# Optimization experiments

Measured on AMD Instinct MI355X. Metric: run time of the kernel, lower is better.

## Reference

```python
import jax, jax.numpy as jnp
import numpy as np

D = 1024      # d_model
H = 16        # num_heads
DH = D // H   # head_dim = 64
BASE = 10000.0


def setup_inputs() -> dict:
    key = jax.random.key(0)
    ks = jax.random.split(key, 5)
    lengths = np.array([1024, 768, 896, 1024], dtype=np.int32)
    cu = np.concatenate([[0], np.cumsum(lengths)]).astype(np.int32)
    T = int(cu[-1])  # 3712 packed tokens
    x = jax.random.normal(ks[0], (T, D), dtype=jnp.float32)
    Wqkv = jax.random.normal(ks[1], (D, 3 * D), dtype=jnp.float32) / np.sqrt(D)
    bqkv = jax.random.normal(ks[2], (3 * D,), dtype=jnp.float32) * 0.02
    Wo = jax.random.normal(ks[3], (D, D), dtype=jnp.float32) / np.sqrt(D)
    bo = jax.random.normal(ks[4], (D,), dtype=jnp.float32) * 0.02
    return {"x": x, "Wqkv": Wqkv, "bqkv": bqkv, "Wo": Wo, "bo": bo,
            "cu_seqlens": jnp.asarray(cu), "max_seqlen": 1024}


def reference(x, Wqkv, bqkv, Wo, bo, cu_seqlens, max_seqlen):
    T = x.shape[0]
    B = cu_seqlens.shape[0] - 1
    S = int(max_seqlen)

    # fused qkv projection: [T, 3, H, DH]
    qkv = (x @ Wqkv + bqkv).reshape(T, 3, H, DH)
    q, k, v = qkv[:, 0], qkv[:, 1], qkv[:, 2]

    # per-token sequence id and within-sequence position (RoPE resets per seq)
    tok = jnp.arange(T)
    seq_id = jnp.searchsorted(cu_seqlens, tok, side='right') - 1  # [T]
    pos = tok - cu_seqlens[seq_id]                                # [T]

    # RoPE, non-interleaved (rotate-half over full head_dim)
    inv_freq = 1.0 / (BASE ** (jnp.arange(0, DH, 2, dtype=jnp.float32) / DH))
    ang = pos[:, None].astype(jnp.float32) * inv_freq             # [T, DH/2]
    cos = jnp.cos(ang)[:, None, :]                                # [T, 1, DH/2]
    sin = jnp.sin(ang)[:, None, :]

    def rope(t):
        t1, t2 = t[..., : DH // 2], t[..., DH // 2:]
        return jnp.concatenate([t1 * cos - t2 * sin, t2 * cos + t1 * sin], axis=-1)

    q, k = rope(q), rope(k)

    # scatter packed tokens into padded [B, S, H, DH] (varlen attention)
    qp = jnp.zeros((B, S, H, DH), x.dtype).at[seq_id, pos].set(q)
    kp = jnp.zeros((B, S, H, DH), x.dtype).at[seq_id, pos].set(k)
    vp = jnp.zeros((B, S, H, DH), x.dtype).at[seq_id, pos].set(v)
    valid = jnp.zeros((B, S), bool).at[seq_id, pos].set(True)

    scale = 1.0 / np.sqrt(DH)
    scores = jnp.einsum('bqhd,bkhd->bhqk', qp, kp) * scale        # [B,H,S,S]
    causal = jnp.tril(jnp.ones((S, S), bool))
    mask = causal[None, None] & valid[:, None, None, :]
    scores = jnp.where(mask, scores, jnp.asarray(-1e30, scores.dtype))
    attn = jax.nn.softmax(scores, axis=-1)
    op = jnp.einsum('bhqk,bkhd->bqhd', attn, vp)                  # [B,S,H,DH]

    # unpad back to packed layout, then output projection (W_o)
    out = op[seq_id, pos].reshape(T, D)
    return out @ Wo + bo
```

## Files before the change

### kernel.cpp

```cpp
#include <hip/hip_runtime.h>

typedef _Float16 f16;
typedef _Float16 f16x8 __attribute__((ext_vector_type(8)));
typedef _Float16 f16x4 __attribute__((ext_vector_type(4)));
typedef float f32x4 __attribute__((ext_vector_type(4)));

#define MFMA16(a, b, c) __builtin_amdgcn_mfma_f32_16x16x32_f16((a), (b), (c), 0, 0, 0)

typedef __attribute__((address_space(3))) void lds_void;
typedef const __attribute__((address_space(1))) void g_void;
__device__ __forceinline__ void async_copy16(void* lds, const void* g) {
    __builtin_amdgcn_global_load_lds((g_void*)g, (lds_void*)lds, 16, 0, 0);
}

__global__ void cvt_x(const float* __restrict__ in, f16* __restrict__ out, int n) {
    int i4 = (blockIdx.x * 256 + threadIdx.x) * 4;
    if (i4 >= n) return;
    float4 v = *reinterpret_cast<const float4*>(in + i4);
    f16x4 o;
    o[0] = (f16)v.x; o[1] = (f16)v.y; o[2] = (f16)v.z; o[3] = (f16)v.w;
    *reinterpret_cast<f16x4*>(out + i4) = o;
}

__global__ void wtrans2(const float* __restrict__ Wqkv, const float* __restrict__ Wo,
                        f16* __restrict__ outQkv, f16* __restrict__ outWo) {
    __shared__ f16 tile[64][65];
    int id = blockIdx.x;
    const float* in; f16* out; int N, bx, by;
    if (id < 768) { in = Wqkv; out = outQkv; N = 3072; bx = id % 48; by = id / 48; }
    else { id -= 768; in = Wo; out = outWo; N = 1024; bx = id % 16; by = id / 16; }
    const int K = 1024;
    int n0 = bx * 64, k0 = by * 64;
    int c = threadIdx.x & 63, rb = threadIdx.x >> 6;
#pragma unroll
    for (int it = 0; it < 16; ++it) {
        int r = rb + it * 4;
        tile[r][c] = (f16)in[(size_t)(k0 + r) * N + n0 + c];
    }
    __syncthreads();
#pragma unroll
    for (int it = 0; it < 16; ++it) {
        int rr = rb + it * 4;
        out[(size_t)(n0 + rr) * K + k0 + c] = tile[c][rr];
    }
}

#define BM 128
#define BN 128
#define BKK 32
__global__ __launch_bounds__(256) void gemm_tile(
    const f16* __restrict__ A, const f16* __restrict__ Bt,
    const float* __restrict__ bias, f16* __restrict__ Ch, float* __restrict__ Cf,
    int M, int N, int K, int nbx) {
    __shared__ f16 lA[2][BM * BKK];
    __shared__ f16 lB[2][BN * BKK];
    int tid = threadIdx.x;
    int lane = tid & 63, w = tid >> 6;
    int lr = lane & 15, lg = lane >> 4;
    int wm = (w & 1) * 64, wn = (w >> 1) * 64;

    int nwg = gridDim.x, wg = blockIdx.x;
    int tile = ((nwg & 7) == 0) ? ((wg & 7) * (nwg >> 3) + (wg >> 3)) : wg;
    int by = tile / nbx, bx = tile % nbx;

    int srow = tid >> 2;
    int scol = (tid & 3) * 8;
    const f16* ga0 = A  + (size_t)min(by * BM + srow,      M - 1) * K + scol;
    const f16* ga1 = A  + (size_t)min(by * BM + 64 + srow, M - 1) * K + scol;
    const f16* gb0 = Bt + (size_t)min(bx * BN + srow,      N - 1) * K + scol;
    const f16* gb1 = Bt + (size_t)min(bx * BN + 64 + srow, N - 1) * K + scol;

    f32x4 acc[4][4] = {};
    int NT = K / BKK;

#define STAGE(curb, kt) do {                                        \
        int ko = (kt) * BKK;                                        \
        async_copy16(&lA[curb][w * 512],        ga0 + ko);          \
        async_copy16(&lA[curb][2048 + w * 512], ga1 + ko);          \
        async_copy16(&lB[curb][w * 512],        gb0 + ko);          \
        async_copy16(&lB[curb][2048 + w * 512], gb1 + ko);          \
    } while (0)

    STAGE(0, 0);
    __syncthreads();
    int cur = 0;
    for (int kt = 0; kt < NT; ++kt) {
        if (kt + 1 < NT) STAGE(cur ^ 1, kt + 1);
        f16x8 af[4], bf[4];
#pragma unroll
        for (int i = 0; i < 4; ++i) {
            af[i] = *reinterpret_cast<const f16x8*>(&lA[cur][(wm + i * 16 + lr) * BKK + lg * 8]);
            bf[i] = *reinterpret_cast<const f16x8*>(&lB[cur][(wn + i * 16 + lr) * BKK + lg * 8]);
        }
#pragma unroll
        for (int mi = 0; mi < 4; ++mi)
#pragma unroll
            for (int ni = 0; ni < 4; ++ni)
                acc[mi][ni] = MFMA16(af[mi], bf[ni], acc[mi][ni]);
        __syncthreads();
        cur ^= 1;
    }
#undef STAGE

#pragma unroll
    for (int mi = 0; mi < 4; ++mi) {
#pragma unroll
        for (int ni = 0; ni < 4; ++ni) {
            int col = bx * BN + wn + ni * 16 + lr;
            float bv = bias ? bias[col] : 0.f;
#pragma unroll
            for (int r = 0; r < 4; ++r) {
                int row = by * BM + wm + mi * 16 + 4 * lg + r;
                if (row >= M) continue;
                float v = acc[mi][ni][r] + bv;
                if (Ch) Ch[(size_t)row * N + col] = (f16)v;
                else    Cf[(size_t)row * N + col] = v;
            }
        }
    }
}

__global__ __launch_bounds__(256) void rope_v(
    const f16* __restrict__ qkv, const int* __restrict__ cu,
    int Bn, int T, int Spad,
    f16* __restrict__ qh2, f16* __restrict__ kh2, f16* __restrict__ vt) {
    __shared__ f16 tile[64][65];
    int h = blockIdx.y;
    int t0 = blockIdx.x * 64;
    int tid = threadIdx.x;
    int c = tid & 63, rb = tid >> 6;
#pragma unroll
    for (int it = 0; it < 16; ++it) {
        int r = rb + it * 4;
        int t = t0 + r;
        f16 v = (f16)0.f;
        if (t < T) v = qkv[(size_t)t * 3072 + 2048 + h * 64 + c];
        tile[r][c] = v;
    }
    int tok = t0 + (tid >> 2);
    int g = tid & 3;
    if (tok < T) {
        int b = 0, pos = tok;
        for (int q = 0; q < Bn; ++q) {
            int lo = cu[q], hi = cu[q + 1];
            if (tok >= lo && tok < hi) { b = q; pos = tok - lo; break; }
        }
        const f16* qp = qkv + (size_t)tok * 3072 + h * 64 + g * 8;
        f16x8 q1 = *reinterpret_cast<const f16x8*>(qp);
        f16x8 q2 = *reinterpret_cast<const f16x8*>(qp + 32);
        f16x8 k1 = *reinterpret_cast<const f16x8*>(qp + 1024);
        f16x8 k2 = *reinterpret_cast<const f16x8*>(qp + 1056);
        f16x8 qo1, qo2, ko1, ko2;
#pragma unroll
        for (int e = 0; e < 8; ++e) {
            int i = g * 8 + e;
            float inv = exp2f((float)i * (-13.287712379549449f / 32.f));
            float ang = (float)pos * inv;
            float sn, cs;
            __sincosf(ang, &sn, &cs);
            float a = (float)q1[e], bq = (float)q2[e];
            float ka = (float)k1[e], kb = (float)k2[e];
            qo1[e] = (f16)((a * cs - bq * sn) * 0.125f);
            qo2[e] = (f16)((bq * cs + a * sn) * 0.125f);
            ko1[e] = (f16)(ka * cs - kb * sn);
            ko2[e] = (f16)(kb * cs + ka * sn);
        }
        size_t ob = ((size_t)(b * 16 + h) * Spad + pos) * 64 + g * 8;
        *reinterpret_cast<f16x8*>(qh2 + ob)      = qo1;
        *reinterpret_cast<f16x8*>(qh2 + ob + 32) = qo2;
        *reinterpret_cast<f16x8*>(kh2 + ob)      = ko1;
        *reinterpret_cast<f16x8*>(kh2 + ob + 32) = ko2;
    }
    __syncthreads();
    int t = t0 + c;
    int bb = 0, pos2 = -1;
    if (t < T) {
        for (int q = 0; q < Bn; ++q) {
            int lo = cu[q], hi = cu[q + 1];
            if (t >= lo && t < hi) { bb = q; pos2 = t - lo; }
        }
    }
#pragma unroll
    for (int it = 0; it < 16; ++it) {
        int d = rb + it * 4;
        if (pos2 >= 0) vt[((size_t)(bb * 16 + h) * 64 + d) * Spad + pos2] = tile[c][d];
    }
}

__global__ __launch_bounds__(64) void attn_fwd(
    const f16* __restrict__ qh2, const f16* __restrict__ kh2,
    const f16* __restrict__ vt, const int* __restrict__ cu,
    f16* __restrict__ oh, int Spad, int nq, int Bn) {
    int wgid = blockIdx.x;
    int nbh = Bn * 16;
    int b, h, qi;
    if ((nbh & 7) == 0) {
        int xcd = wgid & 7, rest = wgid >> 3, nbh8 = nbh >> 3;
        int bhhi = rest % nbh8;
        qi = (nq - 1) - rest / nbh8;
        int bhv = (bhhi << 3) | xcd;
        b = bhv >> 4; h = bhv & 15;
    } else {
        qi = wgid % nq;
        int bhv = wgid / nq;
        b = bhv >> 4; h = bhv & 15;
    }
    int bh = b * 16 + h;
    int s0 = cu[b];
    int len = cu[b + 1] - s0;
    int q0 = qi * 32;
    if (q0 >= len) return;
    int lane = threadIdx.x & 63, lr = lane & 15, lg = lane >> 4;
    __shared__ f16 pl[2][16][40];

    const f16* qbase = qh2 + (size_t)bh * Spad * 64;
    const f16* kbase = kh2 + (size_t)bh * Spad * 64;
    const f16* vbase = vt  + (size_t)bh * 64 * Spad;

    f16x8 qf[2][2];
#pragma unroll
    for (int qt = 0; qt < 2; ++qt) {
        const f16* qp = qbase + (size_t)(q0 + 16 * qt + lr) * 64 + 8 * lg;
        qf[qt][0] = *reinterpret_cast<const f16x8*>(qp);
        qf[qt][1] = *reinterpret_cast<const f16x8*>(qp + 32);
    }
    float mrun[2] = {-1e30f, -1e30f}, lrun[2] = {0.f, 0.f};
    f32x4 oacc[2][4] = {};

    int kend = min(q0 + 32, len);
    int ntk = (kend + 31) >> 5;

    f16x8 kf[2][2], kn[2][2];
#pragma unroll
    for (int j = 0; j < 2; ++j) {
        const f16* kp = kbase + (size_t)(16 * j + lr) * 64 + 8 * lg;
        kf[j][0] = *reinterpret_cast<const f16x8*>(kp);
        kf[j][1] = *reinterpret_cast<const f16x8*>(kp + 32);
    }

    for (int kt = 0; kt < ntk; ++kt) {
        int kk0 = kt << 5;
        f16x8 vf[4];
#pragma unroll
        for (int dt = 0; dt < 4; ++dt)
            vf[dt] = *reinterpret_cast<const f16x8*>(
                vbase + (size_t)(16 * dt + lr) * Spad + kk0 + 8 * lg);
        f32x4 st[2][2];
#pragma unroll
        for (int qt = 0; qt < 2; ++qt)
#pragma unroll
            for (int j = 0; j < 2; ++j) {
                f32x4 z = {0, 0, 0, 0};
                z = MFMA16(kf[j][0], qf[qt][0], z);
                z = MFMA16(kf[j][1], qf[qt][1], z);
                st[qt][j] = z;
            }
        if (kt + 1 < ntk) {
#pragma unroll
            for (int j = 0; j < 2; ++j) {
                const f16* kp = kbase + (size_t)(kk0 + 32 + 16 * j + lr) * 64 + 8 * lg;
                kn[j][0] = *reinterpret_cast<const f16x8*>(kp);
                kn[j][1] = *reinterpret_cast<const f16x8*>(kp + 32);
            }
        }
#pragma unroll
        for (int qt = 0; qt < 2; ++qt) {
            int qr = q0 + 16 * qt + lr;
            float sv[2][4];
            float mx = -1e30f;
#pragma unroll
            for (int j = 0; j < 2; ++j)
#pragma unroll
                for (int r = 0; r < 4; ++r) {
                    int kc = kk0 + 16 * j + 4 * lg + r;
                    float v = st[qt][j][r];
                    if (kc > qr || kc >= len) v = -1e30f;
                    sv[j][r] = v;
                    mx = fmaxf(mx, v);
                }
            mx = fmaxf(mx, __shfl_xor(mx, 16, 64));
            mx = fmaxf(mx, __shfl_xor(mx, 32, 64));
            float mnew = fmaxf(mrun[qt], mx);
            float al = __expf(mrun[qt] - mnew);
            mrun[qt] = mnew;
            float rs = 0.f;
            f16x4 pk0, pk1;
#pragma unroll
            for (int r = 0; r < 4; ++r) {
                float p0 = __expf(sv[0][r] - mnew);
                float p1 = __expf(sv[1][r] - mnew);
                rs += p0 + p1;
                pk0[r] = (f16)p0;
                pk1[r] = (f16)p1;
            }
            rs += __shfl_xor(rs, 16, 64);
            rs += __shfl_xor(rs, 32, 64);
            lrun[qt] = lrun[qt] * al + rs;
            *reinterpret_cast<f16x4*>(&pl[qt][lr][4 * lg])      = pk0;
            *reinterpret_cast<f16x4*>(&pl[qt][lr][16 + 4 * lg]) = pk1;
#pragma unroll
            for (int dt = 0; dt < 4; ++dt)
#pragma unroll
                for (int r = 0; r < 4; ++r) oacc[qt][dt][r] *= al;
        }
        __syncthreads();
        f16x8 pa0 = *reinterpret_cast<const f16x8*>(&pl[0][lr][8 * lg]);
        f16x8 pa1 = *reinterpret_cast<const f16x8*>(&pl[1][lr][8 * lg]);
#pragma unroll
        for (int dt = 0; dt < 4; ++dt) {
            oacc[0][dt] = MFMA16(vf[dt], pa0, oacc[0][dt]);
            oacc[1][dt] = MFMA16(vf[dt], pa1, oacc[1][dt]);
        }
        __syncthreads();
#pragma unroll
        for (int j = 0; j < 2; ++j) {
            kf[j][0] = kn[j][0];
            kf[j][1] = kn[j][1];
        }
    }
#pragma unroll
    for (int qt = 0; qt < 2; ++qt) {
        int qr = q0 + 16 * qt + lr;
        if (qr >= len) continue;
        float linv = 1.f / lrun[qt];
        f16* orow = oh + (size_t)(s0 + qr) * 1024 + h * 64;
#pragma unroll
        for (int dt = 0; dt < 4; ++dt) {
            f16x4 ov;
#pragma unroll
            for (int r = 0; r < 4; ++r) ov[r] = (f16)(oacc[qt][dt][r] * linv);
            *reinterpret_cast<f16x4*>(orow + 16 * dt + 4 * lg) = ov;
        }
    }
}

extern "C" void kernel_launch(void* const* d_in, const int* in_sizes, int n_in,
                              void* d_out, int out_size, void* d_ws, size_t ws_size,
                              hipStream_t stream) {
    const float* x    = (const float*)d_in[0];
    const float* Wqkv = (const float*)d_in[1];
    const float* bqkv = (const float*)d_in[2];
    const float* Wo   = (const float*)d_in[3];
    const float* bo   = (const float*)d_in[4];
    const int*   cu   = (const int*)d_in[5];

    const int Dm = 1024;
    int T  = in_sizes[0] / Dm;
    int Bn = in_sizes[5] - 1;
    int Spad = 1024;

    auto al = [](size_t v) { return (v + 255) & ~(size_t)255; };
    char* w = (char*)d_ws;
    size_t off = 0;
    f16* xh     = (f16*)(w + off); off = al(off + (size_t)2 * T * 1024);
    f16* qkvh   = (f16*)(w + off); off = al(off + (size_t)2 * T * 3072);
    f16* wqkvT  = (f16*)(w + off); off = al(off + (size_t)2 * 3072 * 1024);
    f16* woT    = (f16*)(w + off); off = al(off + (size_t)2 * 1024 * 1024);
    f16* qh2    = (f16*)(w + off); off = al(off + (size_t)2 * Bn * 16 * 64 * (size_t)Spad);
    f16* kh2    = (f16*)(w + off); off = al(off + (size_t)2 * Bn * 16 * 64 * (size_t)Spad);
    f16* vtp    = (f16*)(w + off); off = al(off + (size_t)2 * Bn * 16 * 64 * (size_t)Spad);
    f16* ohp    = (f16*)(w + off); off = al(off + (size_t)2 * T * 1024);
    (void)ws_size;

    {
        int n = T * 1024;
        cvt_x<<<(n / 4 + 255) / 256, 256, 0, stream>>>(x, xh, n);
    }
    wtrans2<<<768 + 256, 256, 0, stream>>>(Wqkv, Wo, wqkvT, woT);
    {
        int nbx = 3072 / BN, nby = (T + BM - 1) / BM;
        gemm_tile<<<nbx * nby, 256, 0, stream>>>(xh, wqkvT, bqkv, qkvh, nullptr, T, 3072, 1024, nbx);
    }
    rope_v<<<dim3((T + 63) / 64, 16), 256, 0, stream>>>(qkvh, cu, Bn, T, Spad, qh2, kh2, vtp);
    {
        int nq = Spad / 32;
        int ngrid = nq * 16 * Bn;
        attn_fwd<<<ngrid, 64, 0, stream>>>(qh2, kh2, vtp, cu, ohp, Spad, nq, Bn);
    }
    {
        int nbx = 1024 / BN, nby = (T + BM - 1) / BM;
        gemm_tile<<<nbx * nby, 256, 0, stream>>>(ohp, woT, bo, nullptr, (float*)d_out, T, 1024, 1024, nbx);
    }
}
```

Baseline: 138.8 us.

## Precompute RoPE trig table and shrink attention query tile to 16 rows

Adds a kernel that builds a cos/sin table per position and frequency, so the RoPE kernel loads those values instead of computing exp2 and sincos per element. The attention kernel now handles 16 query rows per workgroup instead of 32, which doubles the grid and gives finer load balance across the causal triangle. The cost is that each K/V tile is loaded by twice as many workgroups, and there is one extra kernel launch. With the key tile still 32 wide, each workgroup's last tile is half masked more often.

```diff
diff --git a/kernel.cpp b/kernel.cpp
--- a/kernel.cpp
+++ b/kernel.cpp
@@ -20,6 +20,16 @@
     f16x4 o;
     o[0] = (f16)v.x; o[1] = (f16)v.y; o[2] = (f16)v.z; o[3] = (f16)v.w;
     *reinterpret_cast<f16x4*>(out + i4) = o;
+}
+
+__global__ void trig_tab(float2* __restrict__ tab, int Spad) {
+    int idx = blockIdx.x * 256 + threadIdx.x;
+    if (idx >= Spad * 32) return;
+    int pos = idx >> 5, i = idx & 31;
+    float inv = exp2f((float)i * (-13.287712379549449f / 32.f));
+    float sn, cs;
+    __sincosf((float)pos * inv, &sn, &cs);
+    tab[idx] = make_float2(cs, sn);
 }
 
 __global__ void wtrans2(const float* __restrict__ Wqkv, const float* __restrict__ Wo,
@@ -122,7 +132,7 @@
 
 __global__ __launch_bounds__(256) void rope_v(
     const f16* __restrict__ qkv, const int* __restrict__ cu,
-    int Bn, int T, int Spad,
+    const float2* __restrict__ tab, int Bn, int T, int Spad,
     f16* __restrict__ qh2, f16* __restrict__ kh2, f16* __restrict__ vt) {
     __shared__ f16 tile[64][65];
     int h = blockIdx.y;
@@ -150,14 +160,12 @@
         f16x8 q2 = *reinterpret_cast<const f16x8*>(qp + 32);
         f16x8 k1 = *reinterpret_cast<const f16x8*>(qp + 1024);
         f16x8 k2 = *reinterpret_cast<const f16x8*>(qp + 1056);
+        const float2* tb = tab + pos * 32 + g * 8;
         f16x8 qo1, qo2, ko1, ko2;
 #pragma unroll
         for (int e = 0; e < 8; ++e) {
-            int i = g * 8 + e;
-            float inv = exp2f((float)i * (-13.287712379549449f / 32.f));
-            float ang = (float)pos * inv;
-            float sn, cs;
-            __sincosf(ang, &sn, &cs);
+            float2 csn = tb[e];
+            float cs = csn.x, sn = csn.y;
             float a = (float)q1[e], bq = (float)q2[e];
             float ka = (float)k1[e], kb = (float)k2[e];
             qo1[e] = (f16)((a * cs - bq * sn) * 0.125f);
@@ -208,26 +216,25 @@
     int bh = b * 16 + h;
     int s0 = cu[b];
     int len = cu[b + 1] - s0;
-    int q0 = qi * 32;
+    int q0 = qi * 16;
     if (q0 >= len) return;
     int lane = threadIdx.x & 63, lr = lane & 15, lg = lane >> 4;
-    __shared__ f16 pl[2][16][40];
+    __shared__ f16 pl[16][40];
 
     const f16* qbase = qh2 + (size_t)bh * Spad * 64;
     const f16* kbase = kh2 + (size_t)bh * Spad * 64;
     const f16* vbase = vt  + (size_t)bh * 64 * Spad;
 
-    f16x8 qf[2][2];
-#pragma unroll
-    for (int qt = 0; qt < 2; ++qt) {
-        const f16* qp = qbase + (size_t)(q0 + 16 * qt + lr) * 64 + 8 * lg;
-        qf[qt][0] = *reinterpret_cast<const f16x8*>(qp);
-        qf[qt][1] = *reinterpret_cast<const f16x8*>(qp + 32);
-    }
-    float mrun[2] = {-1e30f, -1e30f}, lrun[2] = {0.f, 0.f};
-    f32x4 oacc[2][4] = {};
-
-    int kend = min(q0 + 32, len);
+    f16x8 qf0, qf1;
+    {
+        const f16* qp = qbase + (size_t)(q0 + lr) * 64 + 8 * lg;
+        qf0 = *reinterpret_cast<const f16x8*>(qp);
+        qf1 = *reinterpret_cast<const f16x8*>(qp + 32);
+    }
+    float mrun = -1e30f, lrun = 0.f;
+    f32x4 oacc[4] = {};
+
+    int kend = min(q0 + 16, len);
     int ntk = (kend + 31) >> 5;
 
     f16x8 kf[2][2], kn[2][2];
@@ -245,16 +252,14 @@
         for (int dt = 0; dt < 4; ++dt)
             vf[dt] = *reinterpret_cast<const f16x8*>(
                 vbase + (size_t)(16 * dt + lr) * Spad + kk0 + 8 * lg);
-        f32x4 st[2][2];
-#pragma unroll
-        for (int qt = 0; qt < 2; ++qt)
-#pragma unroll
-            for (int j = 0; j < 2; ++j) {
-                f32x4 z = {0, 0, 0, 0};
-                z = MFMA16(kf[j][0], qf[qt][0], z);
-                z = MFMA16(kf[j][1], qf[qt][1], z);
-                st[qt][j] = z;
-            }
+        f32x4 st[2];
+#pragma unroll
+        for (int j = 0; j < 2; ++j) {
+            f32x4 z = {0, 0, 0, 0};
+            z = MFMA16(kf[j][0], qf0, z);
+            z = MFMA16(kf[j][1], qf1, z);
+            st[j] = z;
+        }
         if (kt + 1 < ntk) {
 #pragma unroll
             for (int j = 0; j < 2; ++j) {
@@ -263,9 +268,8 @@
                 kn[j][1] = *reinterpret_cast<const f16x8*>(kp + 32);
             }
         }
-#pragma unroll
-        for (int qt = 0; qt < 2; ++qt) {
-            int qr = q0 + 16 * qt + lr;
+        {
+            int qr = q0 + lr;
             float sv[2][4];
             float mx = -1e30f;
 #pragma unroll
@@ -273,16 +277,16 @@
 #pragma unroll
                 for (int r = 0; r < 4; ++r) {
                     int kc = kk0 + 16 * j + 4 * lg + r;
-                    float v = st[qt][j][r];
+                    float v = st[j][r];
                     if (kc > qr || kc >= len) v = -1e30f;
                     sv[j][r] = v;
                     mx = fmaxf(mx, v);
                 }
             mx = fmaxf(mx, __shfl_xor(mx, 16, 64));
             mx = fmaxf(mx, __shfl_xor(mx, 32, 64));
-            float mnew = fmaxf(mrun[qt], mx);
-            float al = __expf(mrun[qt] - mnew);
-            mrun[qt] = mnew;
+            float mnew = fmaxf(mrun, mx);
+            float al = __expf(mrun - mnew);
+            mrun = mnew;
             float rs = 0.f;
             f16x4 pk0, pk1;
 #pragma unroll
@@ -295,22 +299,19 @@
             }
             rs += __shfl_xor(rs, 16, 64);
             rs += __shfl_xor(rs, 32, 64);
-            lrun[qt] = lrun[qt] * al + rs;
-            *reinterpret_cast<f16x4*>(&pl[qt][lr][4 * lg])      = pk0;
-            *reinterpret_cast<f16x4*>(&pl[qt][lr][16 + 4 * lg]) = pk1;
+            lrun = lrun * al + rs;
+            *reinterpret_cast<f16x4*>(&pl[lr][4 * lg])      = pk0;
+            *reinterpret_cast<f16x4*>(&pl[lr][16 + 4 * lg]) = pk1;
 #pragma unroll
             for (int dt = 0; dt < 4; ++dt)
 #pragma unroll
-                for (int r = 0; r < 4; ++r) oacc[qt][dt][r] *= al;
+                for (int r = 0; r < 4; ++r) oacc[dt][r] *= al;
         }
         __syncthreads();
-        f16x8 pa0 = *reinterpret_cast<const f16x8*>(&pl[0][lr][8 * lg]);
-        f16x8 pa1 = *reinterpret_cast<const f16x8*>(&pl[1][lr][8 * lg]);
-#pragma unroll
-        for (int dt = 0; dt < 4; ++dt) {
-            oacc[0][dt] = MFMA16(vf[dt], pa0, oacc[0][dt]);
-            oacc[1][dt] = MFMA16(vf[dt], pa1, oacc[1][dt]);
-        }
+        f16x8 pa = *reinterpret_cast<const f16x8*>(&pl[lr][8 * lg]);
+#pragma unroll
+        for (int dt = 0; dt < 4; ++dt)
+            oacc[dt] = MFMA16(vf[dt], pa, oacc[dt]);
         __syncthreads();
 #pragma unroll
         for (int j = 0; j < 2; ++j) {
@@ -318,18 +319,18 @@
             kf[j][1] = kn[j][1];
         }
     }
-#pragma unroll
-    for (int qt = 0; qt < 2; ++qt) {
-        int qr = q0 + 16 * qt + lr;
-        if (qr >= len) continue;
-        float linv = 1.f / lrun[qt];
-        f16* orow = oh + (size_t)(s0 + qr) * 1024 + h * 64;
-#pragma unroll
-        for (int dt = 0; dt < 4; ++dt) {
-            f16x4 ov;
-#pragma unroll
-            for (int r = 0; r < 4; ++r) ov[r] = (f16)(oacc[qt][dt][r] * linv);
-            *reinterpret_cast<f16x4*>(orow + 16 * dt + 4 * lg) = ov;
+    {
+        int qr = q0 + lr;
+        if (qr < len) {
+            float linv = 1.f / lrun;
+            f16* orow = oh + (size_t)(s0 + qr) * 1024 + h * 64;
+#pragma unroll
+            for (int dt = 0; dt < 4; ++dt) {
+                f16x4 ov;
+#pragma unroll
+                for (int r = 0; r < 4; ++r) ov[r] = (f16)(oacc[dt][r] * linv);
+                *reinterpret_cast<f16x4*>(orow + 16 * dt + 4 * lg) = ov;
+            }
         }
     }
 }
@@ -360,20 +361,22 @@
     f16* kh2    = (f16*)(w + off); off = al(off + (size_t)2 * Bn * 16 * 64 * (size_t)Spad);
     f16* vtp    = (f16*)(w + off); off = al(off + (size_t)2 * Bn * 16 * 64 * (size_t)Spad);
     f16* ohp    = (f16*)(w + off); off = al(off + (size_t)2 * T * 1024);
+    float2* tab = (float2*)(w + off); off = al(off + (size_t)8 * Spad * 32);
     (void)ws_size;
 
     {
         int n = T * 1024;
         cvt_x<<<(n / 4 + 255) / 256, 256, 0, stream>>>(x, xh, n);
     }
+    trig_tab<<<(Spad * 32 + 255) / 256, 256, 0, stream>>>(tab, Spad);
     wtrans2<<<768 + 256, 256, 0, stream>>>(Wqkv, Wo, wqkvT, woT);
     {
         int nbx = 3072 / BN, nby = (T + BM - 1) / BM;
         gemm_tile<<<nbx * nby, 256, 0, stream>>>(xh, wqkvT, bqkv, qkvh, nullptr, T, 3072, 1024, nbx);
     }
-    rope_v<<<dim3((T + 63) / 64, 16), 256, 0, stream>>>(qkvh, cu, Bn, T, Spad, qh2, kh2, vtp);
-    {
-        int nq = Spad / 32;
+    rope_v<<<dim3((T + 63) / 64, 16), 256, 0, stream>>>(qkvh, cu, tab, Bn, T, Spad, qh2, kh2, vtp);
+    {
+        int nq = Spad / 16;
         int ngrid = nq * 16 * Bn;
         attn_fwd<<<ngrid, 64, 0, stream>>>(qh2, kh2, vtp, cu, ohp, Spad, nq, Bn);
     }
```

After: 163.1 us. 1.17x slower.

## Split attention KV loop across two waves and precompute RoPE trig table

Applied to the files above, without the earlier changes.

Attention blocks now use two wavefronts that process alternating 32-key tiles, each with its own softmax state and P buffer, then merge partial outputs through shared memory at the end. Block-wide barriers inside the key loop are replaced by per-wave LDS waits. This is meant to halve the serial key-loop length per block and raise latency hiding. Separately, RoPE cos/sin values are precomputed into a table by a new small kernel instead of being recomputed with sincos per token. The cost is an extra kernel launch, extra LDS, and an end-of-block merge step.

```diff
diff --git a/kernel.cpp b/kernel.cpp
--- a/kernel.cpp
+++ b/kernel.cpp
@@ -20,6 +20,16 @@
     f16x4 o;
     o[0] = (f16)v.x; o[1] = (f16)v.y; o[2] = (f16)v.z; o[3] = (f16)v.w;
     *reinterpret_cast<f16x4*>(out + i4) = o;
+}
+
+__global__ void trig_tab(float2* __restrict__ tab, int Spad) {
+    int idx = blockIdx.x * 256 + threadIdx.x;
+    if (idx >= Spad * 32) return;
+    int pos = idx >> 5, i = idx & 31;
+    float inv = exp2f((float)i * (-13.287712379549449f / 32.f));
+    float sn, cs;
+    __sincosf((float)pos * inv, &sn, &cs);
+    tab[idx] = make_float2(cs, sn);
 }
 
 __global__ void wtrans2(const float* __restrict__ Wqkv, const float* __restrict__ Wo,
@@ -122,7 +132,7 @@
 
 __global__ __launch_bounds__(256) void rope_v(
     const f16* __restrict__ qkv, const int* __restrict__ cu,
-    int Bn, int T, int Spad,
+    const float2* __restrict__ tab, int Bn, int T, int Spad,
     f16* __restrict__ qh2, f16* __restrict__ kh2, f16* __restrict__ vt) {
     __shared__ f16 tile[64][65];
     int h = blockIdx.y;
@@ -150,14 +160,12 @@
         f16x8 q2 = *reinterpret_cast<const f16x8*>(qp + 32);
         f16x8 k1 = *reinterpret_cast<const f16x8*>(qp + 1024);
         f16x8 k2 = *reinterpret_cast<const f16x8*>(qp + 1056);
+        const float2* tb = tab + pos * 32 + g * 8;
         f16x8 qo1, qo2, ko1, ko2;
 #pragma unroll
         for (int e = 0; e < 8; ++e) {
-            int i = g * 8 + e;
-            float inv = exp2f((float)i * (-13.287712379549449f / 32.f));
-            float ang = (float)pos * inv;
-            float sn, cs;
-            __sincosf(ang, &sn, &cs);
+            float2 csn = tb[e];
+            float cs = csn.x, sn = csn.y;
             float a = (float)q1[e], bq = (float)q2[e];
             float ka = (float)k1[e], kb = (float)k2[e];
             qo1[e] = (f16)((a * cs - bq * sn) * 0.125f);
@@ -187,7 +195,7 @@
     }
 }
 
-__global__ __launch_bounds__(64) void attn_fwd(
+__global__ __launch_bounds__(128) void attn_fwd(
     const f16* __restrict__ qh2, const f16* __restrict__ kh2,
     const f16* __restrict__ vt, const int* __restrict__ cu,
     f16* __restrict__ oh, int Spad, int nq, int Bn) {
@@ -210,8 +218,12 @@
     int len = cu[b + 1] - s0;
     int q0 = qi * 32;
     if (q0 >= len) return;
-    int lane = threadIdx.x & 63, lr = lane & 15, lg = lane >> 4;
-    __shared__ f16 pl[2][16][40];
+    int tid = threadIdx.x;
+    int wv = tid >> 6;
+    int lane = tid & 63, lr = lane & 15, lg = lane >> 4;
+    __shared__ f16 pl[2][2][16][40];
+    __shared__ float mlb[2][2][16];
+    __shared__ f32x4 owb[2][4][16][4];
 
     const f16* qbase = qh2 + (size_t)bh * Spad * 64;
     const f16* kbase = kh2 + (size_t)bh * Spad * 64;
@@ -233,12 +245,12 @@
     f16x8 kf[2][2], kn[2][2];
 #pragma unroll
     for (int j = 0; j < 2; ++j) {
-        const f16* kp = kbase + (size_t)(16 * j + lr) * 64 + 8 * lg;
+        const f16* kp = kbase + (size_t)(wv * 32 + 16 * j + lr) * 64 + 8 * lg;
         kf[j][0] = *reinterpret_cast<const f16x8*>(kp);
         kf[j][1] = *reinterpret_cast<const f16x8*>(kp + 32);
     }
 
-    for (int kt = 0; kt < ntk; ++kt) {
+    for (int kt = wv; kt < ntk; kt += 2) {
         int kk0 = kt << 5;
         f16x8 vf[4];
 #pragma unroll
@@ -255,10 +267,10 @@
                 z = MFMA16(kf[j][1], qf[qt][1], z);
                 st[qt][j] = z;
             }
-        if (kt + 1 < ntk) {
+        if (kt + 2 < ntk) {
 #pragma unroll
             for (int j = 0; j < 2; ++j) {
-                const f16* kp = kbase + (size_t)(kk0 + 32 + 16 * j + lr) * 64 + 8 * lg;
+                const f16* kp = kbase + (size_t)(kk0 + 64 + 16 * j + lr) * 64 + 8 * lg;
                 kn[j][0] = *reinterpret_cast<const f16x8*>(kp);
                 kn[j][1] = *reinterpret_cast<const f16x8*>(kp + 32);
             }
@@ -296,40 +308,60 @@
             rs += __shfl_xor(rs, 16, 64);
             rs += __shfl_xor(rs, 32, 64);
             lrun[qt] = lrun[qt] * al + rs;
-            *reinterpret_cast<f16x4*>(&pl[qt][lr][4 * lg])      = pk0;
-            *reinterpret_cast<f16x4*>(&pl[qt][lr][16 + 4 * lg]) = pk1;
+            *reinterpret_cast<f16x4*>(&pl[wv][qt][lr][4 * lg])      = pk0;
+            *reinterpret_cast<f16x4*>(&pl[wv][qt][lr][16 + 4 * lg]) = pk1;
 #pragma unroll
             for (int dt = 0; dt < 4; ++dt)
 #pragma unroll
                 for (int r = 0; r < 4; ++r) oacc[qt][dt][r] *= al;
         }
-        __syncthreads();
-        f16x8 pa0 = *reinterpret_cast<const f16x8*>(&pl[0][lr][8 * lg]);
-        f16x8 pa1 = *reinterpret_cast<const f16x8*>(&pl[1][lr][8 * lg]);
+        asm volatile("s_waitcnt lgkmcnt(0)" ::: "memory");
+        __builtin_amdgcn_sched_barrier(0);
+        f16x8 pa0 = *reinterpret_cast<const f16x8*>(&pl[wv][0][lr][8 * lg]);
+        f16x8 pa1 = *reinterpret_cast<const f16x8*>(&pl[wv][1][lr][8 * lg]);
 #pragma unroll
         for (int dt = 0; dt < 4; ++dt) {
             oacc[0][dt] = MFMA16(vf[dt], pa0, oacc[0][dt]);
             oacc[1][dt] = MFMA16(vf[dt], pa1, oacc[1][dt]);
         }
-        __syncthreads();
+        asm volatile("" ::: "memory");
 #pragma unroll
         for (int j = 0; j < 2; ++j) {
             kf[j][0] = kn[j][0];
             kf[j][1] = kn[j][1];
         }
     }
-#pragma unroll
-    for (int qt = 0; qt < 2; ++qt) {
-        int qr = q0 + 16 * qt + lr;
-        if (qr >= len) continue;
-        float linv = 1.f / lrun[qt];
-        f16* orow = oh + (size_t)(s0 + qr) * 1024 + h * 64;
-#pragma unroll
-        for (int dt = 0; dt < 4; ++dt) {
-            f16x4 ov;
-#pragma unroll
-            for (int r = 0; r < 4; ++r) ov[r] = (f16)(oacc[qt][dt][r] * linv);
-            *reinterpret_cast<f16x4*>(orow + 16 * dt + 4 * lg) = ov;
+
+    if (wv == 1) {
+#pragma unroll
+        for (int qt = 0; qt < 2; ++qt) {
+            if (lg == 0) { mlb[qt][0][lr] = mrun[qt]; mlb[qt][1][lr] = lrun[qt]; }
+#pragma unroll
+            for (int dt = 0; dt < 4; ++dt)
+                owb[qt][dt][lr][lg] = oacc[qt][dt];
+        }
+    }
+    __syncthreads();
+    if (wv == 0) {
+#pragma unroll
+        for (int qt = 0; qt < 2; ++qt) {
+            int qr = q0 + 16 * qt + lr;
+            if (qr >= len) continue;
+            float m1 = mlb[qt][0][lr], l1 = mlb[qt][1][lr];
+            float mnew = fmaxf(mrun[qt], m1);
+            float a0 = __expf(mrun[qt] - mnew);
+            float a1 = __expf(m1 - mnew);
+            float linv = 1.f / (lrun[qt] * a0 + l1 * a1);
+            f16* orow = oh + (size_t)(s0 + qr) * 1024 + h * 64;
+#pragma unroll
+            for (int dt = 0; dt < 4; ++dt) {
+                f32x4 o1 = owb[qt][dt][lr][lg];
+                f16x4 ov;
+#pragma unroll
+                for (int r = 0; r < 4; ++r)
+                    ov[r] = (f16)((oacc[qt][dt][r] * a0 + o1[r] * a1) * linv);
+                *reinterpret_cast<f16x4*>(orow + 16 * dt + 4 * lg) = ov;
+            }
         }
     }
 }
@@ -360,22 +392,24 @@
     f16* kh2    = (f16*)(w + off); off = al(off + (size_t)2 * Bn * 16 * 64 * (size_t)Spad);
     f16* vtp    = (f16*)(w + off); off = al(off + (size_t)2 * Bn * 16 * 64 * (size_t)Spad);
     f16* ohp    = (f16*)(w + off); off = al(off + (size_t)2 * T * 1024);
+    float2* tab = (float2*)(w + off); off = al(off + (size_t)8 * Spad * 32);
     (void)ws_size;
 
     {
         int n = T * 1024;
         cvt_x<<<(n / 4 + 255) / 256, 256, 0, stream>>>(x, xh, n);
     }
+    trig_tab<<<(Spad * 32 + 255) / 256, 256, 0, stream>>>(tab, Spad);
     wtrans2<<<768 + 256, 256, 0, stream>>>(Wqkv, Wo, wqkvT, woT);
     {
         int nbx = 3072 / BN, nby = (T + BM - 1) / BM;
         gemm_tile<<<nbx * nby, 256, 0, stream>>>(xh, wqkvT, bqkv, qkvh, nullptr, T, 3072, 1024, nbx);
     }
-    rope_v<<<dim3((T + 63) / 64, 16), 256, 0, stream>>>(qkvh, cu, Bn, T, Spad, qh2, kh2, vtp);
+    rope_v<<<dim3((T + 63) / 64, 16), 256, 0, stream>>>(qkvh, cu, tab, Bn, T, Spad, qh2, kh2, vtp);
     {
         int nq = Spad / 32;
         int ngrid = nq * 16 * Bn;
-        attn_fwd<<<ngrid, 64, 0, stream>>>(qh2, kh2, vtp, cu, ohp, Spad, nq, Bn);
+        attn_fwd<<<ngrid, 128, 0, stream>>>(qh2, kh2, vtp, cu, ohp, Spad, nq, Bn);
     }
     {
         int nbx = 1024 / BN, nby = (T + BM - 1) / BM;
```

Result: faster. 132.6 us (-4.5%).
